# Performance work log

Hardware: AMD Instinct MI355X
Metric: run time of the kernel (lower is better)

The kernel has to match this reference:

```python
import jax, jax.numpy as jnp
import numpy as np

N = 50000      # nodes
E = 320000     # edges, sorted by relation, equal sections of E//R
R = 16         # num_rels
B = 8          # num_bases
IN = 256
OUT = 256


def setup_inputs() -> dict:
    key = jax.random.key(0)
    ks = jax.random.split(key, 7)
    feat = jax.random.normal(ks[0], (N, IN), dtype=jnp.float32)
    weight = jax.random.normal(ks[1], (B, IN, OUT), dtype=jnp.float32) * 0.05
    w_comp = jax.random.normal(ks[2], (R, B), dtype=jnp.float32) * 0.3
    loop_weight = jax.random.normal(ks[3], (IN, OUT), dtype=jnp.float32) * 0.05
    h_bias = jnp.zeros((OUT,), dtype=jnp.float32)
    norm = jax.random.uniform(ks[4], (E, 1), dtype=jnp.float32)
    src_idx = jax.random.randint(ks[5], (E,), 0, N)
    dst_idx = jax.random.randint(ks[6], (E,), 0, N)
    # edges sorted by relation type, equal-size sections (static for jit)
    etypes = jnp.repeat(jnp.arange(R), E // R)
    return dict(feat=feat, weight=weight, w_comp=w_comp, loop_weight=loop_weight,
                h_bias=h_bias, norm=norm, src_idx=src_idx, dst_idx=dst_idx,
                etypes=etypes)


def reference(feat, weight, w_comp, loop_weight, h_bias, norm, src_idx, dst_idx, etypes):
    # basis composition: per-relation weight [R, IN, OUT]
    w_rel = (w_comp @ weight.reshape(B, IN * OUT)).reshape(R, IN, OUT)
    # gather src features per edge; edges are grouped by relation (etypes sorted)
    h_src = feat[src_idx].reshape(R, E // R, IN)        # grouped GEMM operand
    msg = jnp.einsum('rei,rio->reo', h_src, w_rel).reshape(E, OUT)
    msg = msg * norm                                     # edge norm scaling
    # scatter-sum aggregation to dst nodes (fn.sum via update_all)
    node_repr = jax.ops.segment_sum(msg, dst_idx, num_segments=N)
    node_repr = node_repr + h_bias + feat @ loop_weight  # bias + self-loop
    return jax.nn.relu(node_repr)
```

## Files before the change

### kernel.cpp

```cpp
#include <hip/hip_runtime.h>

#define N_    50000
#define E_    320000
#define R_    16
#define B_    8
#define IN_   256
#define OUT_  256
#define EPR_  (E_ / R_)
#define MBLK_ 157
#define NBLK_ 391
#define SBLK_ 196

typedef float  f32x16 __attribute__((ext_vector_type(16)));
typedef __bf16 bf16x8 __attribute__((ext_vector_type(8)));

static __device__ __forceinline__ short f2bf(float f) {
  unsigned u = __float_as_uint(f);
  u = (u + 0x7FFFu + ((u >> 16) & 1u)) >> 16;
  return (short)u;
}
static __device__ __forceinline__ float bf2f(unsigned short s) {
  return __uint_as_float(((unsigned)s) << 16);
}

static __device__ __forceinline__ void gl_lds16(const short* g, short* l) {
  __builtin_amdgcn_global_load_lds(
      (const __attribute__((address_space(1))) void*)g,
      (__attribute__((address_space(3))) void*)l, 16, 0, 0);
}

__global__ void prep_kernel(const float* __restrict__ feat, const float* __restrict__ weight,
                            const float* __restrict__ w_comp, const float* __restrict__ loop_w,
                            short* __restrict__ w_relT, short* __restrict__ loopT,
                            short* __restrict__ feat_bf, int* __restrict__ counts) {
  int gid = blockIdx.x * blockDim.x + threadIdx.x;
  int gsz = gridDim.x * blockDim.x;
  for (int idx = gid; idx < R_ * OUT_ * IN_; idx += gsz) {
    int r = idx >> 16, i = (idx >> 8) & 255, o = idx & 255;
    float s = 0.f;
#pragma unroll
    for (int b = 0; b < B_; ++b)
      s += w_comp[r * B_ + b] * weight[(b * IN_ + i) * OUT_ + o];
    w_relT[(r * OUT_ + o) * IN_ + i] = f2bf(s);
  }
  for (int idx = gid; idx < OUT_ * IN_; idx += gsz) {
    int i = idx >> 8, o = idx & 255;
    loopT[o * IN_ + i] = f2bf(loop_w[i * OUT_ + o]);
  }
  for (int idx = gid; idx < (N_ * IN_) / 4; idx += gsz) {
    float4 v = ((const float4*)feat)[idx];
    short4 s4;
    s4.x = f2bf(v.x); s4.y = f2bf(v.y); s4.z = f2bf(v.z); s4.w = f2bf(v.w);
    ((short4*)feat_bf)[idx] = s4;
  }
  for (int idx = gid; idx < N_; idx += gsz) counts[idx] = 0;
}

__global__ void reorder_kernel(const short* __restrict__ w_relT, short* __restrict__ w_relS) {
  int idx = blockIdx.x * 256 + threadIdx.x;
  if (idx >= R_ * OUT_ * IN_) return;
  int r = idx >> 16;
  int rem = idx & 65535;
  int half = rem >> 15;
  int stage = (rem >> 13) & 3;
  int c = (rem >> 3) & 1023;
  int j = rem & 7;
  int scol = c >> 3;
  int q = (c & 7) ^ (scol & 7);
  int o = (half << 7) + scol;
  int i = (stage << 6) + (q << 3) + j;
  w_relS[idx] = w_relT[((r << 8) + o) * IN_ + i];
}

__global__ void hist_kernel(const int* __restrict__ dst_idx, int* __restrict__ counts) {
  int e = blockIdx.x * 256 + threadIdx.x;
  if (e < E_) atomicAdd(&counts[dst_idx[e]], 1);
}

__global__ void scan1_kernel(const int* __restrict__ counts, int* __restrict__ offsets,
                             int* __restrict__ bsum) {
  __shared__ int tmp[256];
  int tid = threadIdx.x;
  int gid = blockIdx.x * 256 + tid;
  int v = (gid < N_) ? counts[gid] : 0;
  tmp[tid] = v;
  __syncthreads();
  for (int d = 1; d < 256; d <<= 1) {
    int add = (tid >= d) ? tmp[tid - d] : 0;
    __syncthreads();
    tmp[tid] += add;
    __syncthreads();
  }
  if (gid < N_) offsets[gid] = tmp[tid] - v;
  if (tid == 255) bsum[blockIdx.x] = tmp[255];
}

__global__ void scan2_kernel(int* __restrict__ bsum) {
  __shared__ int tmp[256];
  int tid = threadIdx.x;
  int v = (tid < SBLK_) ? bsum[tid] : 0;
  tmp[tid] = v;
  __syncthreads();
  for (int d = 1; d < 256; d <<= 1) {
    int add = (tid >= d) ? tmp[tid - d] : 0;
    __syncthreads();
    tmp[tid] += add;
    __syncthreads();
  }
  if (tid < SBLK_) bsum[tid] = tmp[tid] - v;
}

__global__ void scan3_kernel(int* __restrict__ offsets, const int* __restrict__ bsum,
                             int* __restrict__ woff) {
  int gid = blockIdx.x * 256 + threadIdx.x;
  if (gid < N_) {
    int o = offsets[gid] + bsum[blockIdx.x];
    offsets[gid] = o;
    woff[gid] = o;
  }
}

__global__ void scatter_kernel(const int* __restrict__ dst_idx, int* __restrict__ woff,
                               int* __restrict__ pos) {
  int e = blockIdx.x * 256 + threadIdx.x;
  if (e < E_) {
    int p = atomicAdd(&woff[dst_idx[e]], 1);
    pos[e] = p;
  }
}

template <int MODE>
__launch_bounds__(256)
__global__ void edge_kernel(const short* __restrict__ feat_bf, const short* __restrict__ w_relS,
                            const float* __restrict__ norm, const int* __restrict__ src_idx,
                            const int* __restrict__ dst_idx, const int* __restrict__ pos,
                            short* __restrict__ msg, float* __restrict__ acc_out) {
  __shared__ short lds_b[2][128 * 64];
  int bid  = blockIdx.x;
  int r    = bid / (MBLK_ * 2);
  int rem  = bid - r * (MBLK_ * 2);
  int mblk = rem >> 1, nhalf = rem & 1;
  int e0   = r * EPR_ + mblk * 128;
  int rows = EPR_ - mblk * 128; if (rows > 128) rows = 128;

  int tid = threadIdx.x;
  int lane = tid & 63, wave = tid >> 6;
  int lm = lane & 31, hi = lane >> 5;
  int wr = wave << 5;

  int erow = wr + lm;
  int eg   = e0 + (erow < rows ? erow : 0);
  int src  = src_idx[eg];
  const bf16x8* __restrict__ arow = (const bf16x8*)(feat_bf + (size_t)src * IN_);

  bf16x8 a[16];
#pragma unroll
  for (int i = 0; i < 16; ++i) a[i] = arow[2 * i + hi];

  const short* wt = w_relS + (size_t)(((r << 1) + nhalf) << 2) * 8192;
#pragma unroll
  for (int st = 0; st < 2; ++st) {
#pragma unroll
    for (int j = 0; j < 4; ++j) {
      int chunk = (wave << 2) + j;
      gl_lds16(wt + st * 8192 + chunk * 512 + lane * 8, &lds_b[st][chunk * 512]);
    }
  }

  f32x16 acc[4];
#pragma unroll
  for (int g = 0; g < 4; ++g)
#pragma unroll
    for (int t = 0; t < 16; ++t) acc[g][t] = 0.f;

  __syncthreads();

#pragma unroll
  for (int stage = 0; stage < 4; ++stage) {
    const short* lb = lds_b[stage & 1];
#pragma unroll
    for (int s = 0; s < 4; ++s) {
      bf16x8 af = a[stage * 4 + s];
      int q = s * 2 + hi;
#pragma unroll
      for (int g = 0; g < 4; ++g) {
        int col = (g << 5) + lm;
        bf16x8 bfr = *(const bf16x8*)(&lb[col * 64 + ((q ^ (col & 7)) << 3)]);
        acc[g] = __builtin_amdgcn_mfma_f32_32x32x16_bf16(af, bfr, acc[g], 0, 0, 0);
      }
    }
    __syncthreads();
    if (stage < 2) {
#pragma unroll
      for (int j = 0; j < 4; ++j) {
        int chunk = (wave << 2) + j;
        gl_lds16(wt + (stage + 2) * 8192 + chunk * 512 + lane * 8,
                 &lds_b[stage & 1][chunk * 512]);
      }
    }
  }

  float nr[16]; int er_ok[16]; int prow[16]; int db[16];
#pragma unroll
  for (int t = 0; t < 16; ++t) {
    int row = (t & 3) + ((t >> 2) << 3) + (hi << 2);
    int er  = wr + row;
    int ee  = e0 + (er < rows ? er : 0);
    nr[t]    = norm[ee];
    er_ok[t] = (er < rows);
    prow[t]  = (MODE == 0) ? pos[ee] : 0;
    db[t]    = dst_idx[ee] * OUT_;
  }
#pragma unroll
  for (int g = 0; g < 4; ++g) {
    int col = nhalf * 128 + (g << 5) + lm;
#pragma unroll
    for (int t = 0; t < 16; ++t) {
      if (er_ok[t]) {
        float v = acc[g][t] * nr[t];
        if (MODE == 0)
          __builtin_nontemporal_store(f2bf(v), &msg[(size_t)prow[t] * OUT_ + col]);
        else
          unsafeAtomicAdd(&acc_out[(size_t)db[t] + col], v);
      }
    }
  }
}

__launch_bounds__(256)
__global__ void agg_kernel(const short* __restrict__ msg, const int* __restrict__ offsets,
                           const int* __restrict__ counts, float* __restrict__ out) {
  int n = blockIdx.x * 4 + (threadIdx.x >> 6);
  if (n >= N_) return;
  int lane = threadIdx.x & 63;
  int off = offsets[n], cnt = counts[n];
  float4 a = make_float4(0.f, 0.f, 0.f, 0.f);
  const unsigned long long* __restrict__ m8 = (const unsigned long long*)msg;
  for (int j = 0; j < cnt; ++j) {
    unsigned long long v = __builtin_nontemporal_load(&m8[(size_t)(off + j) * 64 + lane]);
    a.x += bf2f((unsigned short)(v & 0xffffu));
    a.y += bf2f((unsigned short)((v >> 16) & 0xffffu));
    a.z += bf2f((unsigned short)((v >> 32) & 0xffffu));
    a.w += bf2f((unsigned short)(v >> 48));
  }
  ((float4*)out)[(size_t)n * 64 + lane] = a;
}

__global__ void zero_out_kernel(float* __restrict__ out) {
  int idx = blockIdx.x * 256 + threadIdx.x;
  if (idx < N_ * OUT_ / 4)
    ((float4*)out)[idx] = make_float4(0.f, 0.f, 0.f, 0.f);
}

__launch_bounds__(256)
__global__ void selfloop_kernel(const short* __restrict__ feat_bf, const short* __restrict__ loopT,
                                const float* __restrict__ h_bias, float* __restrict__ inout) {
  __shared__ short lds_b[128 * 64];
  int bid = blockIdx.x;
  int mblk = bid >> 1, nhalf = bid & 1;
  int n0 = mblk << 7;
  int rows = N_ - n0; if (rows > 128) rows = 128;

  int tid = threadIdx.x;
  int lane = tid & 63, wave = tid >> 6;
  int lm = lane & 31, hi = lane >> 5;
  int wr = wave << 5;

  int nrow = wr + lm;
  int ng = n0 + (nrow < rows ? nrow : 0);
  const bf16x8* __restrict__ arow = (const bf16x8*)(feat_bf + (size_t)ng * IN_);
  const short*  __restrict__ wb   = loopT + nhalf * 128 * IN_;

  f32x16 acc[4];
#pragma unroll
  for (int g = 0; g < 4; ++g)
#pragma unroll
    for (int t = 0; t < 16; ++t) acc[g][t] = 0.f;

  int scol = tid >> 1, sh = tid & 1;
  const bf16x8* __restrict__ gsrc0 = (const bf16x8*)(wb + scol * IN_ + sh * 32);

  for (int stage = 0; stage < 4; ++stage) {
#pragma unroll
    for (int c8 = 0; c8 < 4; ++c8) {
      int q = sh * 4 + c8;
      bf16x8 v = gsrc0[stage * 8 + c8];
      *(bf16x8*)(&lds_b[scol * 64 + ((q ^ (scol & 7)) << 3)]) = v;
    }
    bf16x8 af[4];
#pragma unroll
    for (int s = 0; s < 4; ++s) af[s] = arow[stage * 8 + s * 2 + hi];
    __syncthreads();
#pragma unroll
    for (int s = 0; s < 4; ++s) {
      int q = s * 2 + hi;
#pragma unroll
      for (int g = 0; g < 4; ++g) {
        int col = (g << 5) + lm;
        bf16x8 bfr = *(const bf16x8*)(&lds_b[col * 64 + ((q ^ (col & 7)) << 3)]);
        acc[g] = __builtin_amdgcn_mfma_f32_32x32x16_bf16(af[s], bfr, acc[g], 0, 0, 0);
      }
    }
    __syncthreads();
  }

#pragma unroll
  for (int g = 0; g < 4; ++g) {
    int col = nhalf * 128 + (g << 5) + lm;
    float hb = h_bias[col];
#pragma unroll
    for (int t = 0; t < 16; ++t) {
      int row = (t & 3) + ((t >> 2) << 3) + (hi << 2);
      int nn = wr + row;
      if (nn < rows) {
        size_t off = (size_t)(n0 + nn) * OUT_ + col;
        float x = inout[off] + acc[g][t] + hb;
        inout[off] = x > 0.f ? x : 0.f;
      }
    }
  }
}

extern "C" void kernel_launch(void* const* d_in, const int* in_sizes, int n_in,
                              void* d_out, int out_size, void* d_ws, size_t ws_size,
                              hipStream_t stream) {
  const float* feat    = (const float*)d_in[0];
  const float* weight  = (const float*)d_in[1];
  const float* w_comp  = (const float*)d_in[2];
  const float* loop_w  = (const float*)d_in[3];
  const float* h_bias  = (const float*)d_in[4];
  const float* norm    = (const float*)d_in[5];
  const int*   src_idx = (const int*)d_in[6];
  const int*   dst_idx = (const int*)d_in[7];
  float* out = (float*)d_out;

  short* w_relT  = (short*)d_ws;
  short* w_relS  = w_relT + R_ * OUT_ * IN_;
  short* loopT   = w_relS + R_ * OUT_ * IN_;
  short* feat_bf = loopT + OUT_ * IN_;
  int*   counts  = (int*)(feat_bf + (size_t)N_ * IN_);
  int*   offsets = counts + N_;
  int*   woff    = offsets + N_;
  int*   bsum    = woff + N_;
  int*   pos     = bsum + 256;
  short* msg     = (short*)(pos + E_);
  size_t need    = (size_t)((char*)(msg + (size_t)E_ * OUT_) - (char*)d_ws);

  prep_kernel<<<1024, 256, 0, stream>>>(feat, weight, w_comp, loop_w,
                                        w_relT, loopT, feat_bf, counts);
  reorder_kernel<<<(R_ * OUT_ * IN_) / 256, 256, 0, stream>>>(w_relT, w_relS);

  if (ws_size >= need) {
    hist_kernel<<<(E_ + 255) / 256, 256, 0, stream>>>(dst_idx, counts);
    scan1_kernel<<<SBLK_, 256, 0, stream>>>(counts, offsets, bsum);
    scan2_kernel<<<1, 256, 0, stream>>>(bsum);
    scan3_kernel<<<SBLK_, 256, 0, stream>>>(offsets, bsum, woff);
    scatter_kernel<<<(E_ + 255) / 256, 256, 0, stream>>>(dst_idx, woff, pos);
    edge_kernel<0><<<MBLK_ * 2 * R_, 256, 0, stream>>>(feat_bf, w_relS, norm, src_idx, dst_idx,
                                                       pos, msg, nullptr);
    agg_kernel<<<(N_ + 3) / 4, 256, 0, stream>>>(msg, offsets, counts, out);
  } else {
    zero_out_kernel<<<(N_ * OUT_ / 4 + 255) / 256, 256, 0, stream>>>(out);
    edge_kernel<1><<<MBLK_ * 2 * R_, 256, 0, stream>>>(feat_bf, w_relS, norm, src_idx, dst_idx,
                                                       nullptr, nullptr, out);
  }

  selfloop_kernel<<<NBLK_ * 2, 256, 0, stream>>>(feat_bf, loopT, h_bias, out);
}
```

Before: 262.6 us.

## Fold self-loop GEMM into edge kernel, sort edges by source block, remap workgroups

The self-loop matmul now runs as a 17th relation inside the edge kernel. Its output goes into the message buffer as one extra slot per node, so the aggregation kernel applies bias and ReLU directly and the separate self-loop pass and its read-modify-write of the output disappear. Edges within each relation are counting-sorted by source block (src>>7) to improve locality of the feature gathers. Workgroup IDs are remapped across 8 groups (likely XCDs). The cost is extra histogram, scan and scatter work, an added indirection through esort, and a larger message buffer.

```diff
diff --git a/kernel.cpp b/kernel.cpp
--- a/kernel.cpp
+++ b/kernel.cpp
@@ -9,7 +9,11 @@
 #define EPR_  (E_ / R_)
 #define MBLK_ 157
 #define NBLK_ 391
-#define SBLK_ 196
+#define NB_   391
+#define KTOT_ (R_ * NB_)
+#define SCN_  (N_ + KTOT_)
+#define SCB_  220
+#define TIL_  (R_ * MBLK_ + NBLK_)
 
 typedef float  f32x16 __attribute__((ext_vector_type(16)));
 typedef __bf16 bf16x8 __attribute__((ext_vector_type(8)));
@@ -31,8 +35,8 @@
 
 __global__ void prep_kernel(const float* __restrict__ feat, const float* __restrict__ weight,
                             const float* __restrict__ w_comp, const float* __restrict__ loop_w,
-                            short* __restrict__ w_relT, short* __restrict__ loopT,
-                            short* __restrict__ feat_bf, int* __restrict__ counts) {
+                            short* __restrict__ w_relT, short* __restrict__ feat_bf,
+                            int* __restrict__ counts, int* __restrict__ counts2) {
   int gid = blockIdx.x * blockDim.x + threadIdx.x;
   int gsz = gridDim.x * blockDim.x;
   for (int idx = gid; idx < R_ * OUT_ * IN_; idx += gsz) {
@@ -45,7 +49,7 @@
   }
   for (int idx = gid; idx < OUT_ * IN_; idx += gsz) {
     int i = idx >> 8, o = idx & 255;
-    loopT[o * IN_ + i] = f2bf(loop_w[i * OUT_ + o]);
+    w_relT[((R_ * OUT_) + o) * IN_ + i] = f2bf(loop_w[i * OUT_ + o]);
   }
   for (int idx = gid; idx < (N_ * IN_) / 4; idx += gsz) {
     float4 v = ((const float4*)feat)[idx];
@@ -54,11 +58,12 @@
     ((short4*)feat_bf)[idx] = s4;
   }
   for (int idx = gid; idx < N_; idx += gsz) counts[idx] = 0;
+  for (int idx = gid; idx < KTOT_; idx += gsz) counts2[idx] = 0;
 }
 
 __global__ void reorder_kernel(const short* __restrict__ w_relT, short* __restrict__ w_relS) {
   int idx = blockIdx.x * 256 + threadIdx.x;
-  if (idx >= R_ * OUT_ * IN_) return;
+  if (idx >= (R_ + 1) * OUT_ * IN_) return;
   int r = idx >> 16;
   int rem = idx & 65535;
   int half = rem >> 15;
@@ -72,17 +77,22 @@
   w_relS[idx] = w_relT[((r << 8) + o) * IN_ + i];
 }
 
-__global__ void hist_kernel(const int* __restrict__ dst_idx, int* __restrict__ counts) {
+__global__ void hist_kernel(const int* __restrict__ dst_idx, const int* __restrict__ src_idx,
+                            int* __restrict__ counts, int* __restrict__ counts2) {
   int e = blockIdx.x * 256 + threadIdx.x;
-  if (e < E_) atomicAdd(&counts[dst_idx[e]], 1);
-}
-
-__global__ void scan1_kernel(const int* __restrict__ counts, int* __restrict__ offsets,
-                             int* __restrict__ bsum) {
+  if (e < E_) {
+    atomicAdd(&counts[dst_idx[e]], 1);
+    int r = e / EPR_;
+    atomicAdd(&counts2[r * NB_ + (src_idx[e] >> 7)], 1);
+  }
+}
+
+__global__ void scan1_kernel(const int* __restrict__ counts, const int* __restrict__ counts2,
+                             int* __restrict__ offc, int* __restrict__ bsum) {
   __shared__ int tmp[256];
   int tid = threadIdx.x;
   int gid = blockIdx.x * 256 + tid;
-  int v = (gid < N_) ? counts[gid] : 0;
+  int v = (gid < N_) ? counts[gid] + 1 : (gid < SCN_ ? counts2[gid - N_] : 0);
   tmp[tid] = v;
   __syncthreads();
   for (int d = 1; d < 256; d <<= 1) {
@@ -91,14 +101,14 @@
     tmp[tid] += add;
     __syncthreads();
   }
-  if (gid < N_) offsets[gid] = tmp[tid] - v;
+  if (gid < SCN_) offc[gid] = tmp[tid] - v;
   if (tid == 255) bsum[blockIdx.x] = tmp[255];
 }
 
 __global__ void scan2_kernel(int* __restrict__ bsum) {
   __shared__ int tmp[256];
   int tid = threadIdx.x;
-  int v = (tid < SBLK_) ? bsum[tid] : 0;
+  int v = (tid < SCB_) ? bsum[tid] : 0;
   tmp[tid] = v;
   __syncthreads();
   for (int d = 1; d < 256; d <<= 1) {
@@ -107,25 +117,29 @@
     tmp[tid] += add;
     __syncthreads();
   }
-  if (tid < SBLK_) bsum[tid] = tmp[tid] - v;
-}
-
-__global__ void scan3_kernel(int* __restrict__ offsets, const int* __restrict__ bsum,
-                             int* __restrict__ woff) {
+  if (tid < SCB_) bsum[tid] = tmp[tid] - v;
+}
+
+__global__ void scan3_kernel(int* __restrict__ offc, const int* __restrict__ bsum,
+                             int* __restrict__ woffc) {
   int gid = blockIdx.x * 256 + threadIdx.x;
-  if (gid < N_) {
-    int o = offsets[gid] + bsum[blockIdx.x];
-    offsets[gid] = o;
-    woff[gid] = o;
-  }
-}
-
-__global__ void scatter_kernel(const int* __restrict__ dst_idx, int* __restrict__ woff,
-                               int* __restrict__ pos) {
+  if (gid < SCN_) {
+    int o = offc[gid] + bsum[blockIdx.x];
+    offc[gid] = o;
+    woffc[gid] = o + (gid < N_ ? 1 : 0);
+  }
+}
+
+__global__ void scatter_kernel(const int* __restrict__ dst_idx, const int* __restrict__ src_idx,
+                               int* __restrict__ woffc, int* __restrict__ pos,
+                               int* __restrict__ esort) {
   int e = blockIdx.x * 256 + threadIdx.x;
   if (e < E_) {
-    int p = atomicAdd(&woff[dst_idx[e]], 1);
-    pos[e] = p;
+    pos[e] = atomicAdd(&woffc[dst_idx[e]], 1);
+    int r = e / EPR_;
+    int k = r * NB_ + (src_idx[e] >> 7);
+    int s = atomicAdd(&woffc[N_ + k], 1) - (E_ + N_);
+    esort[s] = e;
   }
 }
 
@@ -133,15 +147,22 @@
 __launch_bounds__(256)
 __global__ void edge_kernel(const short* __restrict__ feat_bf, const short* __restrict__ w_relS,
                             const float* __restrict__ norm, const int* __restrict__ src_idx,
-                            const int* __restrict__ dst_idx, const int* __restrict__ pos,
+                            const int* __restrict__ dst_idx, const int* __restrict__ esort,
+                            const int* __restrict__ pos, const int* __restrict__ offc,
                             short* __restrict__ msg, float* __restrict__ acc_out) {
   __shared__ short lds_b[2][128 * 64];
-  int bid  = blockIdx.x;
-  int r    = bid / (MBLK_ * 2);
-  int rem  = bid - r * (MBLK_ * 2);
-  int mblk = rem >> 1, nhalf = rem & 1;
-  int e0   = r * EPR_ + mblk * 128;
-  int rows = EPR_ - mblk * 128; if (rows > 128) rows = 128;
+  const int nwg = TIL_ * 2;
+  int xx = blockIdx.x & 7, oo = blockIdx.x >> 3;
+  const int q = nwg >> 3, rr = nwg & 7;
+  int wgid = (xx < rr ? xx * (q + 1) : rr * (q + 1) + (xx - rr) * q) + oo;
+  int tile = wgid >> 1, nhalf = wgid & 1;
+  int r, mblk;
+  if (tile < R_ * MBLK_) { r = tile / MBLK_; mblk = tile - r * MBLK_; }
+  else                   { r = R_;           mblk = tile - R_ * MBLK_; }
+  const bool self = (r == R_);
+  int base = self ? mblk * 128 : r * EPR_ + mblk * 128;
+  int lim  = self ? N_ - mblk * 128 : EPR_ - mblk * 128;
+  int rows = lim > 128 ? 128 : lim;
 
   int tid = threadIdx.x;
   int lane = tid & 63, wave = tid >> 6;
@@ -149,8 +170,8 @@
   int wr = wave << 5;
 
   int erow = wr + lm;
-  int eg   = e0 + (erow < rows ? erow : 0);
-  int src  = src_idx[eg];
+  int eg   = base + (erow < rows ? erow : 0);
+  int src  = self ? eg : src_idx[esort[eg]];
   const bf16x8* __restrict__ arow = (const bf16x8*)(feat_bf + (size_t)src * IN_);
 
   bf16x8 a[16];
@@ -181,11 +202,11 @@
 #pragma unroll
     for (int s = 0; s < 4; ++s) {
       bf16x8 af = a[stage * 4 + s];
-      int q = s * 2 + hi;
+      int qq = s * 2 + hi;
 #pragma unroll
       for (int g = 0; g < 4; ++g) {
         int col = (g << 5) + lm;
-        bf16x8 bfr = *(const bf16x8*)(&lb[col * 64 + ((q ^ (col & 7)) << 3)]);
+        bf16x8 bfr = *(const bf16x8*)(&lb[col * 64 + ((qq ^ (col & 7)) << 3)]);
         acc[g] = __builtin_amdgcn_mfma_f32_32x32x16_bf16(af, bfr, acc[g], 0, 0, 0);
       }
     }
@@ -205,11 +226,18 @@
   for (int t = 0; t < 16; ++t) {
     int row = (t & 3) + ((t >> 2) << 3) + (hi << 2);
     int er  = wr + row;
-    int ee  = e0 + (er < rows ? er : 0);
-    nr[t]    = norm[ee];
+    int ee  = base + (er < rows ? er : 0);
     er_ok[t] = (er < rows);
-    prow[t]  = (MODE == 0) ? pos[ee] : 0;
-    db[t]    = dst_idx[ee] * OUT_;
+    if (self) {
+      nr[t] = 1.f;
+      prow[t] = offc[ee];
+      db[t] = ee * OUT_;
+    } else {
+      int em = esort[ee];
+      nr[t]   = norm[em];
+      prow[t] = (MODE == 0) ? pos[em] : 0;
+      db[t]   = dst_idx[em] * OUT_;
+    }
   }
 #pragma unroll
   for (int g = 0; g < 4; ++g) {
@@ -228,12 +256,13 @@
 }
 
 __launch_bounds__(256)
-__global__ void agg_kernel(const short* __restrict__ msg, const int* __restrict__ offsets,
-                           const int* __restrict__ counts, float* __restrict__ out) {
+__global__ void agg_kernel(const short* __restrict__ msg, const int* __restrict__ offc,
+                           const int* __restrict__ counts, const float* __restrict__ h_bias,
+                           float* __restrict__ out) {
   int n = blockIdx.x * 4 + (threadIdx.x >> 6);
   if (n >= N_) return;
   int lane = threadIdx.x & 63;
-  int off = offsets[n], cnt = counts[n];
+  int off = offc[n], cnt = counts[n] + 1;
   float4 a = make_float4(0.f, 0.f, 0.f, 0.f);
   const unsigned long long* __restrict__ m8 = (const unsigned long long*)msg;
   for (int j = 0; j < cnt; ++j) {
@@ -243,6 +272,11 @@
     a.z += bf2f((unsigned short)((v >> 32) & 0xffffu));
     a.w += bf2f((unsigned short)(v >> 48));
   }
+  float4 b = ((const float4*)h_bias)[lane];
+  a.x = fmaxf(a.x + b.x, 0.f);
+  a.y = fmaxf(a.y + b.y, 0.f);
+  a.z = fmaxf(a.z + b.z, 0.f);
+  a.w = fmaxf(a.w + b.w, 0.f);
   ((float4*)out)[(size_t)n * 64 + lane] = a;
 }
 
@@ -251,73 +285,16 @@
   if (idx < N_ * OUT_ / 4)
     ((float4*)out)[idx] = make_float4(0.f, 0.f, 0.f, 0.f);
 }
-
-__launch_bounds__(256)
-__global__ void selfloop_kernel(const short* __restrict__ feat_bf, const short* __restrict__ loopT,
-                                const float* __restrict__ h_bias, float* __restrict__ inout) {
-  __shared__ short lds_b[128 * 64];
-  int bid = blockIdx.x;
-  int mblk = bid >> 1, nhalf = bid & 1;
-  int n0 = mblk << 7;
-  int rows = N_ - n0; if (rows > 128) rows = 128;
-
-  int tid = threadIdx.x;
-  int lane = tid & 63, wave = tid >> 6;
-  int lm = lane & 31, hi = lane >> 5;
-  int wr = wave << 5;
-
-  int nrow = wr + lm;
-  int ng = n0 + (nrow < rows ? nrow : 0);
-  const bf16x8* __restrict__ arow = (const bf16x8*)(feat_bf + (size_t)ng * IN_);
-  const short*  __restrict__ wb   = loopT + nhalf * 128 * IN_;
-
-  f32x16 acc[4];
-#pragma unroll
-  for (int g = 0; g < 4; ++g)
-#pragma unroll
-    for (int t = 0; t < 16; ++t) acc[g][t] = 0.f;
-
-  int scol = tid >> 1, sh = tid & 1;
-  const bf16x8* __restrict__ gsrc0 = (const bf16x8*)(wb + scol * IN_ + sh * 32);
-
-  for (int stage = 0; stage < 4; ++stage) {
-#pragma unroll
-    for (int c8 = 0; c8 < 4; ++c8) {
-      int q = sh * 4 + c8;
-      bf16x8 v = gsrc0[stage * 8 + c8];
-      *(bf16x8*)(&lds_b[scol * 64 + ((q ^ (scol & 7)) << 3)]) = v;
-    }
-    bf16x8 af[4];
-#pragma unroll
-    for (int s = 0; s < 4; ++s) af[s] = arow[stage * 8 + s * 2 + hi];
-    __syncthreads();
-#pragma unroll
-    for (int s = 0; s < 4; ++s) {
-      int q = s * 2 + hi;
-#pragma unroll
-      for (int g = 0; g < 4; ++g) {
-        int col = (g << 5) + lm;
-        bf16x8 bfr = *(const bf16x8*)(&lds_b[col * 64 + ((q ^ (col & 7)) << 3)]);
-        acc[g] = __builtin_amdgcn_mfma_f32_32x32x16_bf16(af[s], bfr, acc[g], 0, 0, 0);
-      }
-    }
-    __syncthreads();
-  }
-
-#pragma unroll
-  for (int g = 0; g < 4; ++g) {
-    int col = nhalf * 128 + (g << 5) + lm;
-    float hb = h_bias[col];
-#pragma unroll
-    for (int t = 0; t < 16; ++t) {
-      int row = (t & 3) + ((t >> 2) << 3) + (hi << 2);
-      int nn = wr + row;
-      if (nn < rows) {
-        size_t off = (size_t)(n0 + nn) * OUT_ + col;
-        float x = inout[off] + acc[g][t] + hb;
-        inout[off] = x > 0.f ? x : 0.f;
-      }
-    }
+__global__ void bias_relu_kernel(float* __restrict__ out, const float* __restrict__ h_bias) {
+  int idx = blockIdx.x * 256 + threadIdx.x;
+  if (idx < N_ * OUT_ / 4) {
+    float4 v = ((float4*)out)[idx];
+    float4 b = ((const float4*)h_bias)[idx & 63];
+    v.x = fmaxf(v.x + b.x, 0.f);
+    v.y = fmaxf(v.y + b.y, 0.f);
+    v.z = fmaxf(v.z + b.z, 0.f);
+    v.w = fmaxf(v.w + b.w, 0.f);
+    ((float4*)out)[idx] = v;
   }
 }
 
@@ -335,35 +312,35 @@
   float* out = (float*)d_out;
 
   short* w_relT  = (short*)d_ws;
-  short* w_relS  = w_relT + R_ * OUT_ * IN_;
-  short* loopT   = w_relS + R_ * OUT_ * IN_;
-  short* feat_bf = loopT + OUT_ * IN_;
+  short* w_relS  = w_relT + (R_ + 1) * OUT_ * IN_;
+  short* feat_bf = w_relS + (R_ + 1) * OUT_ * IN_;
   int*   counts  = (int*)(feat_bf + (size_t)N_ * IN_);
-  int*   offsets = counts + N_;
-  int*   woff    = offsets + N_;
-  int*   bsum    = woff + N_;
+  int*   counts2 = counts + N_;
+  int*   offc    = counts2 + KTOT_;
+  int*   woffc   = offc + SCN_;
+  int*   bsum    = woffc + SCN_;
   int*   pos     = bsum + 256;
-  short* msg     = (short*)(pos + E_);
-  size_t need    = (size_t)((char*)(msg + (size_t)E_ * OUT_) - (char*)d_ws);
+  int*   esort   = pos + E_;
+  short* msg     = (short*)(esort + E_);
+  size_t need    = (size_t)((char*)(msg + (size_t)(E_ + N_) * OUT_) - (char*)d_ws);
 
   prep_kernel<<<1024, 256, 0, stream>>>(feat, weight, w_comp, loop_w,
-                                        w_relT, loopT, feat_bf, counts);
-  reorder_kernel<<<(R_ * OUT_ * IN_) / 256, 256, 0, stream>>>(w_relT, w_relS);
+                                        w_relT, feat_bf, counts, counts2);
+  reorder_kernel<<<((R_ + 1) * OUT_ * IN_) / 256, 256, 0, stream>>>(w_relT, w_relS);
+  hist_kernel<<<(E_ + 255) / 256, 256, 0, stream>>>(dst_idx, src_idx, counts, counts2);
+  scan1_kernel<<<SCB_, 256, 0, stream>>>(counts, counts2, offc, bsum);
+  scan2_kernel<<<1, 256, 0, stream>>>(bsum);
+  scan3_kernel<<<SCB_, 256, 0, stream>>>(offc, bsum, woffc);
+  scatter_kernel<<<(E_ + 255) / 256, 256, 0, stream>>>(dst_idx, src_idx, woffc, pos, esort);
 
   if (ws_size >= need) {
-    hist_kernel<<<(E_ + 255) / 256, 256, 0, stream>>>(dst_idx, counts);
-    scan1_kernel<<<SBLK_, 256, 0, stream>>>(counts, offsets, bsum);
-    scan2_kernel<<<1, 256, 0, stream>>>(bsum);
-    scan3_kernel<<<SBLK_, 256, 0, stream>>>(offsets, bsum, woff);
-    scatter_kernel<<<(E_ + 255) / 256, 256, 0, stream>>>(dst_idx, woff, pos);
-    edge_kernel<0><<<MBLK_ * 2 * R_, 256, 0, stream>>>(feat_bf, w_relS, norm, src_idx, dst_idx,
-                                                       pos, msg, nullptr);
-    agg_kernel<<<(N_ + 3) / 4, 256, 0, stream>>>(msg, offsets, counts, out);
+    edge_kernel<0><<<TIL_ * 2, 256, 0, stream>>>(feat_bf, w_relS, norm, src_idx, dst_idx,
+                                                 esort, pos, offc, msg, nullptr);
+    agg_kernel<<<(N_ + 3) / 4, 256, 0, stream>>>(msg, offc, counts, h_bias, out);
   } else {
     zero_out_kernel<<<(N_ * OUT_ / 4 + 255) / 256, 256, 0, stream>>>(out);
-    edge_kernel<1><<<MBLK_ * 2 * R_, 256, 0, stream>>>(feat_bf, w_relS, norm, src_idx, dst_idx,
-                                                       nullptr, nullptr, out);
-  }
-
-  selfloop_kernel<<<NBLK_ * 2, 256, 0, stream>>>(feat_bf, loopT, h_bias, out);
-}
+    edge_kernel<1><<<TIL_ * 2, 256, 0, stream>>>(feat_bf, w_relS, norm, src_idx, dst_idx,
+                                                 esort, nullptr, offc, nullptr, out);
+    bias_relu_kernel<<<(N_ * OUT_ / 4 + 255) / 256, 256, 0, stream>>>(out, h_bias);
+  }
+}
```

Result: slower. 274.3 us (+4.4%).
